# Kernel optimization log

Measured on AMD Instinct MI355X. Metric: run time of the kernel, lower is better.

The kernel has to match this reference:

```python
import jax, jax.numpy as jnp
import numpy as np


def setup_inputs() -> dict:
    key = jax.random.key(0)
    ks = jax.random.split(key, 5)
    B, S, D, U = 16, 4096, 256, 256
    scale = 1.0 / np.sqrt(D)
    return {
        "values": jax.random.normal(ks[0], (B, S, D), dtype=jnp.float32),
        "query": jax.random.normal(ks[1], (B, D), dtype=jnp.float32),
        "W1": jax.random.normal(ks[2], (D, U), dtype=jnp.float32) * scale,
        "b1": jnp.zeros((U,), dtype=jnp.float32),
        "W2": jax.random.normal(ks[3], (D, U), dtype=jnp.float32) * scale,
        "b2": jnp.zeros((U,), dtype=jnp.float32),
        "V": jax.random.normal(ks[4], (U, 1), dtype=jnp.float32) * (1.0 / np.sqrt(U)),
        "bV": jnp.zeros((1,), dtype=jnp.float32),
    }


def reference(values, query, W1, b1, W2, b2, V, bV):
    # values: [B, S, D], query: [B, D]
    proj_v = jnp.einsum("bsd,du->bsu", values, W1) + b1          # [B, S, U]
    proj_q = (query @ W2 + b2)[:, None, :]                        # [B, 1, U]
    score = jnp.tanh(proj_v + proj_q) @ V + bV                    # [B, S, 1]
    attention_weights = jax.nn.softmax(score, axis=1)             # [B, S, 1]
    context_vector = jnp.sum(attention_weights * values, axis=1)  # [B, D]
    return context_vector, attention_weights
```

## Files before the change

kernel.cpp:

```cpp
#include <hip/hip_runtime.h>
#include <hip/hip_bf16.h>

#define B 16
#define S 4096
#define D 256
#define U 256
#define ROWS 64
#define NCHK (S / ROWS)

typedef short short8 __attribute__((ext_vector_type(8)));
typedef float f32x4 __attribute__((ext_vector_type(4)));

__device__ __forceinline__ ushort f2bf(float f) {
    union { float f; uint u; } x{f};
    uint r = (x.u + 0x7fffu + ((x.u >> 16) & 1u)) >> 16;
    return (ushort)r;
}

__device__ __forceinline__ float fast_tanh(float x) {
    float e = __expf(2.0f * x);
    return 1.0f - 2.0f * __builtin_amdgcn_rcpf(e + 1.0f);
}

__global__ void ka_setup(const float* __restrict__ query, const float* __restrict__ W2,
                         const float* __restrict__ b2, const float* __restrict__ b1,
                         const float* __restrict__ W1, float* __restrict__ pqb,
                         ushort* __restrict__ W1p) {
    __shared__ float pp[4][U];
    int bid = blockIdx.x, t = threadIdx.x;
    if (bid < 16) {
        const float* qb = query + bid * D;
        int u0 = (t & 63) * 4, dc = t >> 6;
        float4 a = {0.f, 0.f, 0.f, 0.f};
#pragma unroll 16
        for (int i = 0; i < 64; ++i) {
            int d = dc * 64 + i;
            float qd = qb[d];
            float4 wv = *(const float4*)&W2[d * U + u0];
            a.x = fmaf(qd, wv.x, a.x);
            a.y = fmaf(qd, wv.y, a.y);
            a.z = fmaf(qd, wv.z, a.z);
            a.w = fmaf(qd, wv.w, a.w);
        }
        *(float4*)&pp[dc][u0] = a;
        __syncthreads();
        pqb[bid * U + t] = pp[0][t] + pp[1][t] + pp[2][t] + pp[3][t] + b2[t] + b1[t];
    } else {
        int kk = bid - 16;
        int l = t & 63, g = t >> 6;
        int colu0 = l & 15;
        int k0 = kk * 32 + (l >> 4) * 8;
#pragma unroll
        for (int i = 0; i < 4; ++i) {
            int nt = g * 4 + i;
            int colu = nt * 16 + colu0;
            ushort* dst = W1p + (((nt * 8) + kk) * 64 + l) * 8;
#pragma unroll
            for (int e = 0; e < 8; ++e) dst[e] = f2bf(W1[(k0 + e) * U + colu]);
        }
    }
}

__global__ void kb_scores(const float* __restrict__ values, const ushort* __restrict__ W1p,
                          const float* __restrict__ pqb, const float* __restrict__ V,
                          const float* __restrict__ bV, float* __restrict__ cstats,
                          float* __restrict__ cpart, float* __restrict__ wout) {
    __shared__ ushort Alds[ROWS * 256];
    __shared__ float red[4][ROWS];
    __shared__ float wch[ROWS];
    const int bid = blockIdx.x;
    const int t = threadIdx.x;
    const int w = t >> 6, l = t & 63;
    char* lds = (char*)Alds;
    const int b = bid >> 6;
    const int s0 = (bid & 63) * ROWS;

    const float* src = values + ((size_t)(b * S + s0)) * D;
#pragma unroll
    for (int i = 0; i < 16; ++i) {
        int row = i * 4 + w;
        int col = l * 4;
        float4 v = *(const float4*)&src[row * 256 + col];
        ushort4 h;
        h.x = f2bf(v.x); h.y = f2bf(v.y); h.z = f2bf(v.z); h.w = f2bf(v.w);
        int byte = (row * 512 + col * 2) ^ ((row & 7) << 4);
        *(ushort4*)(lds + byte) = h;
    }
    __syncthreads();

    const int lrow = l & 15, lk = l >> 4;
    f32x4 acc[4][4];
#pragma unroll
    for (int mt = 0; mt < 4; ++mt)
#pragma unroll
        for (int nt = 0; nt < 4; ++nt) acc[mt][nt] = (f32x4){0.f, 0.f, 0.f, 0.f};

    for (int kk = 0; kk < 8; ++kk) {
        short8 afr[4], bfr[4];
#pragma unroll
        for (int mt = 0; mt < 4; ++mt) {
            int row = mt * 16 + lrow;
            int byte = (row * 512 + kk * 64 + lk * 16) ^ ((row & 7) << 4);
            afr[mt] = *(const short8*)(lds + byte);
        }
#pragma unroll
        for (int nt = 0; nt < 4; ++nt)
            bfr[nt] = *(const short8*)&W1p[((((w * 4 + nt) * 8) + kk) * 64 + l) * 8];
#pragma unroll
        for (int mt = 0; mt < 4; ++mt)
#pragma unroll
            for (int nt = 0; nt < 4; ++nt)
                acc[mt][nt] = __builtin_amdgcn_mfma_f32_16x16x32_bf16(
                    afr[mt], bfr[nt], acc[mt][nt], 0, 0, 0);
    }

    float bb[4], vv[4];
#pragma unroll
    for (int nt = 0; nt < 4; ++nt) {
        int u = (w * 4 + nt) * 16 + lrow;
        bb[nt] = pqb[b * U + u];
        vv[nt] = V[u];
    }
#pragma unroll
    for (int mt = 0; mt < 4; ++mt) {
#pragma unroll
        for (int r = 0; r < 4; ++r) {
            float s = 0.f;
#pragma unroll
            for (int nt = 0; nt < 4; ++nt)
                s += fast_tanh(acc[mt][nt][r] + bb[nt]) * vv[nt];
            s += __shfl_xor(s, 1);
            s += __shfl_xor(s, 2);
            s += __shfl_xor(s, 4);
            s += __shfl_xor(s, 8);
            if (lrow == 0) red[w][mt * 16 + lk * 4 + r] = s;
        }
    }
    __syncthreads();

    if (t < ROWS) {
        float s = red[0][t] + red[1][t] + red[2][t] + red[3][t] + bV[0];
        float m = s;
#pragma unroll
        for (int off = 32; off; off >>= 1) m = fmaxf(m, __shfl_xor(m, off));
        float z0 = __expf(s - m);
        wch[t] = z0;
        wout[b * S + s0 + t] = z0;
        float z = z0;
#pragma unroll
        for (int off = 32; off; off >>= 1) z += __shfl_xor(z, off);
        if (t == 0) {
            cstats[2 * bid] = m;
            cstats[2 * bid + 1] = z;
        }
    }
    __syncthreads();

    union { uint i; float f; } cv;
    float cacc = 0.f;
#pragma unroll 8
    for (int r = 0; r < ROWS; ++r) {
        int byte = (r * 512 + t * 2) ^ ((r & 7) << 4);
        ushort u = *(const ushort*)(lds + byte);
        cv.i = (uint)u << 16;
        cacc = fmaf(wch[r], cv.f, cacc);
    }
    cpart[(size_t)bid * D + t] = cacc;
}

__global__ void kc_final(const float* __restrict__ cstats, const float* __restrict__ cpart,
                         float* __restrict__ wout, float* __restrict__ ctx) {
    __shared__ float scl[NCHK];
    __shared__ float stats2[2];
    __shared__ float part[4][64];
    int b = blockIdx.x >> 2, q = blockIdx.x & 3;
    int t = threadIdx.x;

    if (t < NCHK) {
        float m = cstats[2 * (b * NCHK + t)];
        float z = cstats[2 * (b * NCHK + t) + 1];
        float M = m;
#pragma unroll
        for (int off = 32; off; off >>= 1) M = fmaxf(M, __shfl_xor(M, off));
        float zz = z * __expf(m - M);
#pragma unroll
        for (int off = 32; off; off >>= 1) zz += __shfl_xor(zz, off);
        scl[t] = __expf(m - M);
        if (t == 0) { stats2[0] = M; stats2[1] = zz; }
    }
    __syncthreads();
    float invZ = 1.0f / stats2[1];

    int tq = t >> 6, dl = t & 63;
    int d = q * 64 + dl;
    float acc = 0.f;
#pragma unroll
    for (int i = 0; i < 16; ++i) {
        int c = tq * 16 + i;
        acc = fmaf(scl[c], cpart[(size_t)(b * NCHK + c) * D + d], acc);
    }
    part[tq][dl] = acc;

#pragma unroll
    for (int i = 0; i < 4; ++i) {
        int ss = q * 1024 + i * 256 + t;
        wout[b * S + ss] *= scl[ss >> 6] * invZ;
    }
    __syncthreads();
    if (t < 64)
        ctx[b * D + q * 64 + t] =
            (part[0][t] + part[1][t] + part[2][t] + part[3][t]) * invZ;
}

extern "C" void kernel_launch(void* const* d_in, const int* in_sizes, int n_in,
                              void* d_out, int out_size, void* d_ws, size_t ws_size,
                              hipStream_t stream) {
    const float* values = (const float*)d_in[0];
    const float* query  = (const float*)d_in[1];
    const float* W1     = (const float*)d_in[2];
    const float* b1     = (const float*)d_in[3];
    const float* W2     = (const float*)d_in[4];
    const float* b2     = (const float*)d_in[5];
    const float* V      = (const float*)d_in[6];
    const float* bV     = (const float*)d_in[7];

    float* out  = (float*)d_out;
    float* ctx  = out;
    float* wout = out + B * D;

    float* ws     = (float*)d_ws;
    float* pqb    = ws;
    float* cstats = pqb + B * U;
    float* cpart  = cstats + 2048;
    ushort* W1p   = (ushort*)(cpart + (size_t)B * NCHK * D);

    ka_setup<<<24, 256, 0, stream>>>(query, W2, b2, b1, W1, pqb, W1p);
    kb_scores<<<B * NCHK, 256, 0, stream>>>(values, W1p, pqb, V, bV,
                                            cstats, cpart, wout);
    kc_final<<<B * 4, 256, 0, stream>>>(cstats, cpart, wout, ctx);
}
```

Before: 46.70 us.

## Load A fragments directly from global per wave, skip LDS staging before MFMA

Instead of cooperatively staging the bf16-converted values tile in LDS and syncing before the GEMM, each wave now reads its A fragments straight from global memory, converts them in registers and feeds MFMA directly. Wave 0 also writes its converted fragments into LDS for the later context reduction. This removes the up-front barrier and LDS round-trip but makes all four waves read the same 64-row tile, quadrupling global/L2 traffic for values. It also redoes the bf16 conversion per wave. A launch bound of 4 blocks per SM is added to constrain registers.

After: 65.46 us. 40.2% more time.

```diff
diff --git a/kernel.cpp b/kernel.cpp
--- a/kernel.cpp
+++ b/kernel.cpp
@@ -61,10 +61,11 @@
     }
 }
 
-__global__ void kb_scores(const float* __restrict__ values, const ushort* __restrict__ W1p,
-                          const float* __restrict__ pqb, const float* __restrict__ V,
-                          const float* __restrict__ bV, float* __restrict__ cstats,
-                          float* __restrict__ cpart, float* __restrict__ wout) {
+__global__ __launch_bounds__(256, 4) void kb_scores(
+    const float* __restrict__ values, const ushort* __restrict__ W1p,
+    const float* __restrict__ pqb, const float* __restrict__ V,
+    const float* __restrict__ bV, float* __restrict__ cstats,
+    float* __restrict__ cpart, float* __restrict__ wout) {
     __shared__ ushort Alds[ROWS * 256];
     __shared__ float red[4][ROWS];
     __shared__ float wch[ROWS];
@@ -74,21 +75,10 @@
     char* lds = (char*)Alds;
     const int b = bid >> 6;
     const int s0 = (bid & 63) * ROWS;
-
-    const float* src = values + ((size_t)(b * S + s0)) * D;
-#pragma unroll
-    for (int i = 0; i < 16; ++i) {
-        int row = i * 4 + w;
-        int col = l * 4;
-        float4 v = *(const float4*)&src[row * 256 + col];
-        ushort4 h;
-        h.x = f2bf(v.x); h.y = f2bf(v.y); h.z = f2bf(v.z); h.w = f2bf(v.w);
-        int byte = (row * 512 + col * 2) ^ ((row & 7) << 4);
-        *(ushort4*)(lds + byte) = h;
-    }
-    __syncthreads();
-
     const int lrow = l & 15, lk = l >> 4;
+
+    const float* vbase = values + ((size_t)(b * S + s0)) * D;
+
     f32x4 acc[4][4];
 #pragma unroll
     for (int mt = 0; mt < 4; ++mt)
@@ -96,22 +86,30 @@
         for (int nt = 0; nt < 4; ++nt) acc[mt][nt] = (f32x4){0.f, 0.f, 0.f, 0.f};
 
     for (int kk = 0; kk < 8; ++kk) {
-        short8 afr[4], bfr[4];
+        short8 bfr[4];
+#pragma unroll
+        for (int nt = 0; nt < 4; ++nt)
+            bfr[nt] = *(const short8*)&W1p[((((w * 4 + nt) * 8) + kk) * 64 + l) * 8];
 #pragma unroll
         for (int mt = 0; mt < 4; ++mt) {
             int row = mt * 16 + lrow;
-            int byte = (row * 512 + kk * 64 + lk * 16) ^ ((row & 7) << 4);
-            afr[mt] = *(const short8*)(lds + byte);
-        }
-#pragma unroll
-        for (int nt = 0; nt < 4; ++nt)
-            bfr[nt] = *(const short8*)&W1p[((((w * 4 + nt) * 8) + kk) * 64 + l) * 8];
-#pragma unroll
-        for (int mt = 0; mt < 4; ++mt)
+            const float* p = vbase + row * 256 + kk * 32 + lk * 8;
+            float4 a0 = *(const float4*)p;
+            float4 a1 = *(const float4*)(p + 4);
+            short8 af;
+            af[0] = (short)f2bf(a0.x); af[1] = (short)f2bf(a0.y);
+            af[2] = (short)f2bf(a0.z); af[3] = (short)f2bf(a0.w);
+            af[4] = (short)f2bf(a1.x); af[5] = (short)f2bf(a1.y);
+            af[6] = (short)f2bf(a1.z); af[7] = (short)f2bf(a1.w);
+            if (w == 0) {
+                int byte = (row * 512 + kk * 64 + lk * 16) ^ ((row & 7) << 4);
+                *(short8*)(lds + byte) = af;
+            }
 #pragma unroll
             for (int nt = 0; nt < 4; ++nt)
                 acc[mt][nt] = __builtin_amdgcn_mfma_f32_16x16x32_bf16(
-                    afr[mt], bfr[nt], acc[mt][nt], 0, 0, 0);
+                    af, bfr[nt], acc[mt][nt], 0, 0, 0);
+        }
     }
 
     float bb[4], vv[4];
```

## Process two chunks per block with register-prefetched double-buffered LDS

Applied to the files above, without the earlier changes.

Each scores block now handles two 64-row chunks. The next chunk's global loads go into registers while the current chunk's MFMA and softmax work runs, and the result is written into a second LDS buffer. This hides global load latency and halves the grid to 512 blocks, at the cost of more registers, double the LDS, and fewer blocks for parallelism. The query projection in the setup kernel is also simplified to a one-thread-per-output loop without shared-memory reduction.

Measured after the change: 83.80 us. 79.4% more time.

```diff
diff --git a/kernel.cpp b/kernel.cpp
--- a/kernel.cpp
+++ b/kernel.cpp
@@ -7,6 +7,7 @@
 #define U 256
 #define ROWS 64
 #define NCHK (S / ROWS)
+#define CPB 2
 
 typedef short short8 __attribute__((ext_vector_type(8)));
 typedef float f32x4 __attribute__((ext_vector_type(4)));
@@ -22,29 +23,19 @@
     return 1.0f - 2.0f * __builtin_amdgcn_rcpf(e + 1.0f);
 }
 
-__global__ void ka_setup(const float* __restrict__ query, const float* __restrict__ W2,
+__global__ void ka_setup(const float* __restrict__ q, const float* __restrict__ W2,
                          const float* __restrict__ b2, const float* __restrict__ b1,
                          const float* __restrict__ W1, float* __restrict__ pqb,
                          ushort* __restrict__ W1p) {
-    __shared__ float pp[4][U];
     int bid = blockIdx.x, t = threadIdx.x;
     if (bid < 16) {
-        const float* qb = query + bid * D;
-        int u0 = (t & 63) * 4, dc = t >> 6;
-        float4 a = {0.f, 0.f, 0.f, 0.f};
-#pragma unroll 16
-        for (int i = 0; i < 64; ++i) {
-            int d = dc * 64 + i;
-            float qd = qb[d];
-            float4 wv = *(const float4*)&W2[d * U + u0];
-            a.x = fmaf(qd, wv.x, a.x);
-            a.y = fmaf(qd, wv.y, a.y);
-            a.z = fmaf(qd, wv.z, a.z);
-            a.w = fmaf(qd, wv.w, a.w);
-        }
-        *(float4*)&pp[dc][u0] = a;
-        __syncthreads();
-        pqb[bid * U + t] = pp[0][t] + pp[1][t] + pp[2][t] + pp[3][t] + b2[t] + b1[t];
+        int b = bid, u = t;
+        const float* qb = q + b * D;
+        float acc = b2[u] + b1[u];
+#pragma unroll 8
+        for (int d = 0; d < D; ++d)
+            acc = fmaf(qb[d], W2[d * U + u], acc);
+        pqb[b * U + u] = acc;
     } else {
         int kk = bid - 16;
         int l = t & 63, g = t >> 6;
@@ -61,58 +52,20 @@
     }
 }
 
-__global__ void kb_scores(const float* __restrict__ values, const ushort* __restrict__ W1p,
-                          const float* __restrict__ pqb, const float* __restrict__ V,
-                          const float* __restrict__ bV, float* __restrict__ cstats,
-                          float* __restrict__ cpart, float* __restrict__ wout) {
-    __shared__ ushort Alds[ROWS * 256];
+__global__ __launch_bounds__(256, 2) void kb_scores(
+    const float* __restrict__ values, const ushort* __restrict__ W1p,
+    const float* __restrict__ pqb, const float* __restrict__ V,
+    const float* __restrict__ bV, float* __restrict__ cstats,
+    float* __restrict__ cpart, float* __restrict__ wout) {
+    __shared__ ushort Alds[2][ROWS * 256];
     __shared__ float red[4][ROWS];
     __shared__ float wch[ROWS];
     const int bid = blockIdx.x;
     const int t = threadIdx.x;
     const int w = t >> 6, l = t & 63;
-    char* lds = (char*)Alds;
-    const int b = bid >> 6;
-    const int s0 = (bid & 63) * ROWS;
-
-    const float* src = values + ((size_t)(b * S + s0)) * D;
-#pragma unroll
-    for (int i = 0; i < 16; ++i) {
-        int row = i * 4 + w;
-        int col = l * 4;
-        float4 v = *(const float4*)&src[row * 256 + col];
-        ushort4 h;
-        h.x = f2bf(v.x); h.y = f2bf(v.y); h.z = f2bf(v.z); h.w = f2bf(v.w);
-        int byte = (row * 512 + col * 2) ^ ((row & 7) << 4);
-        *(ushort4*)(lds + byte) = h;
-    }
-    __syncthreads();
-
     const int lrow = l & 15, lk = l >> 4;
-    f32x4 acc[4][4];
-#pragma unroll
-    for (int mt = 0; mt < 4; ++mt)
-#pragma unroll
-        for (int nt = 0; nt < 4; ++nt) acc[mt][nt] = (f32x4){0.f, 0.f, 0.f, 0.f};
-
-    for (int kk = 0; kk < 8; ++kk) {
-        short8 afr[4], bfr[4];
-#pragma unroll
-        for (int mt = 0; mt < 4; ++mt) {
-            int row = mt * 16 + lrow;
-            int byte = (row * 512 + kk * 64 + lk * 16) ^ ((row & 7) << 4);
-            afr[mt] = *(const short8*)(lds + byte);
-        }
-#pragma unroll
-        for (int nt = 0; nt < 4; ++nt)
-            bfr[nt] = *(const short8*)&W1p[((((w * 4 + nt) * 8) + kk) * 64 + l) * 8];
-#pragma unroll
-        for (int mt = 0; mt < 4; ++mt)
-#pragma unroll
-            for (int nt = 0; nt < 4; ++nt)
-                acc[mt][nt] = __builtin_amdgcn_mfma_f32_16x16x32_bf16(
-                    afr[mt], bfr[nt], acc[mt][nt], 0, 0, 0);
-    }
+    const int chunk0 = bid * CPB;
+    const int b = chunk0 >> 6;
 
     float bb[4], vv[4];
 #pragma unroll
@@ -121,51 +74,124 @@
         bb[nt] = pqb[b * U + u];
         vv[nt] = V[u];
     }
-#pragma unroll
-    for (int mt = 0; mt < 4; ++mt) {
-#pragma unroll
-        for (int r = 0; r < 4; ++r) {
-            float s = 0.f;
+    const float bV0 = bV[0];
+
+    float4 vreg[16];
+    {
+        const float* src = values + ((size_t)(b * S + (chunk0 & 63) * ROWS)) * D;
+#pragma unroll
+        for (int i = 0; i < 16; ++i)
+            vreg[i] = *(const float4*)&src[(i * 4 + w) * 256 + l * 4];
+        char* lds = (char*)Alds[0];
+#pragma unroll
+        for (int i = 0; i < 16; ++i) {
+            int row = i * 4 + w;
+            ushort4 h;
+            h.x = f2bf(vreg[i].x); h.y = f2bf(vreg[i].y);
+            h.z = f2bf(vreg[i].z); h.w = f2bf(vreg[i].w);
+            int byte = (row * 512 + l * 8) ^ ((row & 7) << 4);
+            *(ushort4*)(lds + byte) = h;
+        }
+    }
+
+    for (int c = 0; c < CPB; ++c) {
+        const int chunk = chunk0 + c;
+        const int s0 = (chunk & 63) * ROWS;
+        char* lds = (char*)Alds[c & 1];
+
+        if (c + 1 < CPB) {
+            const float* src = values + ((size_t)(b * S + ((chunk + 1) & 63) * ROWS)) * D;
+#pragma unroll
+            for (int i = 0; i < 16; ++i)
+                vreg[i] = *(const float4*)&src[(i * 4 + w) * 256 + l * 4];
+        }
+        __syncthreads();
+
+        f32x4 acc[4][4];
+#pragma unroll
+        for (int mt = 0; mt < 4; ++mt)
+#pragma unroll
+            for (int nt = 0; nt < 4; ++nt) acc[mt][nt] = (f32x4){0.f, 0.f, 0.f, 0.f};
+
+#pragma unroll
+        for (int kk = 0; kk < 8; ++kk) {
+            short8 afr[4], bfr[4];
 #pragma unroll
             for (int nt = 0; nt < 4; ++nt)
-                s += fast_tanh(acc[mt][nt][r] + bb[nt]) * vv[nt];
-            s += __shfl_xor(s, 1);
-            s += __shfl_xor(s, 2);
-            s += __shfl_xor(s, 4);
-            s += __shfl_xor(s, 8);
-            if (lrow == 0) red[w][mt * 16 + lk * 4 + r] = s;
-        }
-    }
-    __syncthreads();
-
-    if (t < ROWS) {
-        float s = red[0][t] + red[1][t] + red[2][t] + red[3][t] + bV[0];
-        float m = s;
-#pragma unroll
-        for (int off = 32; off; off >>= 1) m = fmaxf(m, __shfl_xor(m, off));
-        float z0 = __expf(s - m);
-        wch[t] = z0;
-        wout[b * S + s0 + t] = z0;
-        float z = z0;
-#pragma unroll
-        for (int off = 32; off; off >>= 1) z += __shfl_xor(z, off);
-        if (t == 0) {
-            cstats[2 * bid] = m;
-            cstats[2 * bid + 1] = z;
-        }
-    }
-    __syncthreads();
-
-    union { uint i; float f; } cv;
-    float cacc = 0.f;
+                bfr[nt] = *(const short8*)&W1p[((((w * 4 + nt) * 8) + kk) * 64 + l) * 8];
+#pragma unroll
+            for (int mt = 0; mt < 4; ++mt) {
+                int row = mt * 16 + lrow;
+                int byte = (row * 512 + kk * 64 + lk * 16) ^ ((row & 7) << 4);
+                afr[mt] = *(const short8*)(lds + byte);
+            }
+#pragma unroll
+            for (int mt = 0; mt < 4; ++mt)
+#pragma unroll
+                for (int nt = 0; nt < 4; ++nt)
+                    acc[mt][nt] = __builtin_amdgcn_mfma_f32_16x16x32_bf16(
+                        afr[mt], bfr[nt], acc[mt][nt], 0, 0, 0);
+        }
+
+#pragma unroll
+        for (int mt = 0; mt < 4; ++mt) {
+#pragma unroll
+            for (int r = 0; r < 4; ++r) {
+                float s = 0.f;
+#pragma unroll
+                for (int nt = 0; nt < 4; ++nt)
+                    s += fast_tanh(acc[mt][nt][r] + bb[nt]) * vv[nt];
+                s += __shfl_xor(s, 1);
+                s += __shfl_xor(s, 2);
+                s += __shfl_xor(s, 4);
+                s += __shfl_xor(s, 8);
+                if (lrow == 0) red[w][mt * 16 + lk * 4 + r] = s;
+            }
+        }
+        __syncthreads();
+
+        if (t < ROWS) {
+            float s = red[0][t] + red[1][t] + red[2][t] + red[3][t] + bV0;
+            float m = s;
+#pragma unroll
+            for (int off = 32; off; off >>= 1) m = fmaxf(m, __shfl_xor(m, off));
+            float z0 = __expf(s - m);
+            wch[t] = z0;
+            wout[b * S + s0 + t] = z0;
+            float z = z0;
+#pragma unroll
+            for (int off = 32; off; off >>= 1) z += __shfl_xor(z, off);
+            if (t == 0) {
+                cstats[2 * chunk] = m;
+                cstats[2 * chunk + 1] = z;
+            }
+        }
+        __syncthreads();
+
+        union { uint i; float f; } cv;
+        float cacc = 0.f;
 #pragma unroll 8
-    for (int r = 0; r < ROWS; ++r) {
-        int byte = (r * 512 + t * 2) ^ ((r & 7) << 4);
-        ushort u = *(const ushort*)(lds + byte);
-        cv.i = (uint)u << 16;
-        cacc = fmaf(wch[r], cv.f, cacc);
-    }
-    cpart[(size_t)bid * D + t] = cacc;
+        for (int r = 0; r < ROWS; ++r) {
+            int byte = (r * 512 + t * 2) ^ ((r & 7) << 4);
+            ushort u = *(const ushort*)(lds + byte);
+            cv.i = (uint)u << 16;
+            cacc = fmaf(wch[r], cv.f, cacc);
+        }
+        cpart[(size_t)chunk * D + t] = cacc;
+
+        if (c + 1 < CPB) {
+            char* ldsn = (char*)Alds[(c + 1) & 1];
+#pragma unroll
+            for (int i = 0; i < 16; ++i) {
+                int row = i * 4 + w;
+                ushort4 h;
+                h.x = f2bf(vreg[i].x); h.y = f2bf(vreg[i].y);
+                h.z = f2bf(vreg[i].z); h.w = f2bf(vreg[i].w);
+                int byte = (row * 512 + l * 8) ^ ((row & 7) << 4);
+                *(ushort4*)(ldsn + byte) = h;
+            }
+        }
+    }
 }
 
 __global__ void kc_final(const float* __restrict__ cstats, const float* __restrict__ cpart,
@@ -232,10 +258,10 @@
     float* pqb    = ws;
     float* cstats = pqb + B * U;
     float* cpart  = cstats + 2048;
-    ushort* W1p   = (ushort*)(cpart + (size_t)B * NCHK * D);
+    ushort* W1p   = (ushort*)(cpart + B * NCHK * D);
 
     ka_setup<<<24, 256, 0, stream>>>(query, W2, b2, b1, W1, pqb, W1p);
-    kb_scores<<<B * NCHK, 256, 0, stream>>>(values, W1p, pqb, V, bV,
-                                            cstats, cpart, wout);
+    kb_scores<<<B * NCHK / CPB, 256, 0, stream>>>(values, W1p, pqb, V, bV,
+                                                  cstats, cpart, wout);
     kc_final<<<B * 4, 256, 0, stream>>>(cstats, cpart, wout, ctx);
 }
```
